# Optimization experiments

Hardware: AMD Instinct MI355X
Metric: run time of the kernel (lower is better)

Reference implementation:

```python
import jax, jax.numpy as jnp
import numpy as np

N_BUCKETS = 512
SLOTS_PER_BUCKET = 32
TAU = 0.1
ALPHA = 0.5


def _l2norm(x, eps=1e-12):
    return x / jnp.maximum(jnp.linalg.norm(x, axis=-1, keepdims=True), eps)


def setup_inputs() -> dict:
    key = jax.random.key(0)
    ks = jax.random.split(key, 6)
    B, T, D = 2, 2048, 1024
    total_slots = N_BUCKETS * SLOTS_PER_BUCKET
    vocab = 50257
    query_emb = jax.random.normal(ks[0], (B, T, D), dtype=jnp.float32)
    tids = jax.random.randint(ks[1], (B, T), 0, vocab)
    slot_keys = jax.random.normal(ks[2], (total_slots, D), dtype=jnp.float32)
    slot_values = jax.random.normal(ks[3], (total_slots, D), dtype=jnp.float32)
    slot_tids = jax.random.randint(ks[4], (total_slots,), 0, vocab)
    centroid_codebook = _l2norm(jax.random.normal(ks[5], (N_BUCKETS, D), dtype=jnp.float32))
    return {
        "query_emb": query_emb,
        "tids": tids,
        "slot_keys": slot_keys,
        "slot_values": slot_values,
        "slot_tids": slot_tids,
        "centroid_codebook": centroid_codebook,
    }


def reference(query_emb, tids, slot_keys, slot_values, slot_tids, centroid_codebook):
    # CentroidAddressableManifold.read
    buckets = tids % N_BUCKETS                                  # [B,T]
    lex_anchors = centroid_codebook[buckets]                    # [B,T,D]
    q_norm = _l2norm(query_emb)
    # bucket-indexed gather of 32 slots per token
    indices = buckets[..., None] * SLOTS_PER_BUCKET + jnp.arange(SLOTS_PER_BUCKET)  # [B,T,S]
    b_keys = slot_keys[indices]                                 # [B,T,S,D]
    b_vals = slot_values[indices]                               # [B,T,S,D]
    unified_query = _l2norm(ALPHA * q_norm + (1.0 - ALPHA) * lex_anchors)
    scores = jnp.einsum("btd,btsd->bts", unified_query, b_keys)  # [B,T,S]
    # hard-match path
    gathered_tids = slot_tids[indices]                          # [B,T,S]
    match_mask = (tids[..., None] == gathered_tids).astype(scores.dtype)
    match_sum = match_mask.sum(axis=-1, keepdims=True)
    has_match = match_sum > 0
    probs_hard = match_mask / (match_sum + 1e-9)
    probs_soft = jax.nn.softmax(scores / TAU, axis=-1)
    val_hard = jnp.einsum("bts,btsw->btw", probs_hard, b_vals)
    val_soft = jnp.einsum("bts,btsw->btw", probs_soft, b_vals)
    val_out = jnp.where(has_match, val_hard, val_soft)          # [B,T,D]
    return val_out
```

## Files before the change

### kernel.cpp

```cpp
#include <hip/hip_runtime.h>

#define NB 512
#define SLOTS 32
#define D 1024
#define D4 256
#define TC 16
#define CAP 64
#define TAU_INV 10.0f
#define BT 512

__global__ void k_zero(int* __restrict__ cnt) {
    if (threadIdx.x < NB) cnt[threadIdx.x] = 0;
}

__global__ void k_build(const int* __restrict__ tids, int n,
                        int* __restrict__ cnt, int* __restrict__ list) {
    int i = blockIdx.x * 256 + threadIdx.x;
    if (i < n) {
        int b = tids[i] & (NB - 1);
        int p = atomicAdd(&cnt[b], 1);
        if (p < CAP) list[b * CAP + p] = i;
    }
}

__global__ __launch_bounds__(BT, 2)
void k_main(const float* __restrict__ query,
            const int*   __restrict__ tids,
            const float* __restrict__ skeys,
            const float* __restrict__ svals,
            const int*   __restrict__ stids,
            const float* __restrict__ centroid,
            float*       __restrict__ out,
            const int*   __restrict__ cnt,
            const int*   __restrict__ list)
{
    const int bucket = blockIdx.x;
    const int tidx   = threadIdx.x;
    const int lane   = tidx & 63;
    const int wid    = tidx >> 6;

    const int count = min(cnt[bucket], CAP);
    if (count == 0) return;

    __shared__ float s_anchor[D];
    __shared__ float s_uq[TC][D];
    __shared__ float s_scores[TC][SLOTS];
    __shared__ float s_probs[TC][SLOTS];
    __shared__ int   s_tok[TC];
    __shared__ int   s_ttid[TC];

    if (tidx < D4)
        ((float4*)s_anchor)[tidx] = ((const float4*)centroid)[bucket * D4 + tidx];
    __syncthreads();

    for (int c0 = 0; c0 < count; c0 += TC) {
        const int nt = min(TC, count - c0);

        for (int t = wid; t < nt; t += 8) {
            const int tok = list[bucket * CAP + c0 + t];
            const float4* q4 = (const float4*)(query + (size_t)tok * D);
            float4 qv[4];
            float ss = 0.f;
            #pragma unroll
            for (int j = 0; j < 4; ++j) {
                qv[j] = q4[lane + 64 * j];
                ss += qv[j].x*qv[j].x + qv[j].y*qv[j].y + qv[j].z*qv[j].z + qv[j].w*qv[j].w;
            }
            #pragma unroll
            for (int off = 32; off >= 1; off >>= 1) ss += __shfl_xor(ss, off);
            const float qn = 0.5f / fmaxf(sqrtf(ss), 1e-12f);

            float4 uv[4];
            float ss2 = 0.f;
            #pragma unroll
            for (int j = 0; j < 4; ++j) {
                float4 av = ((const float4*)s_anchor)[lane + 64 * j];
                uv[j].x = qv[j].x * qn + 0.5f * av.x;
                uv[j].y = qv[j].y * qn + 0.5f * av.y;
                uv[j].z = qv[j].z * qn + 0.5f * av.z;
                uv[j].w = qv[j].w * qn + 0.5f * av.w;
                ss2 += uv[j].x*uv[j].x + uv[j].y*uv[j].y + uv[j].z*uv[j].z + uv[j].w*uv[j].w;
            }
            #pragma unroll
            for (int off = 32; off >= 1; off >>= 1) ss2 += __shfl_xor(ss2, off);
            const float un = 1.0f / fmaxf(sqrtf(ss2), 1e-12f);
            #pragma unroll
            for (int j = 0; j < 4; ++j) {
                float4 w4 = make_float4(uv[j].x*un, uv[j].y*un, uv[j].z*un, uv[j].w*un);
                ((float4*)s_uq[t])[lane + 64 * j] = w4;
            }
            if (lane == 0) { s_tok[t] = tok; s_ttid[t] = tids[tok]; }
        }
        __syncthreads();

        {
            const float4* kr = (const float4*)(skeys + ((size_t)bucket * SLOTS + wid * 4) * D);
            float4 k0[4], k1[4], k2[4], k3[4];
            #pragma unroll
            for (int j = 0; j < 4; ++j) {
                k0[j] = kr[0 * D4 + lane + 64 * j];
                k1[j] = kr[1 * D4 + lane + 64 * j];
                k2[j] = kr[2 * D4 + lane + 64 * j];
                k3[j] = kr[3 * D4 + lane + 64 * j];
            }
            for (int t = 0; t < nt; ++t) {
                const float4* u4 = (const float4*)s_uq[t];
                float P0 = 0.f, P1 = 0.f, P2 = 0.f, P3 = 0.f;
                #pragma unroll
                for (int j = 0; j < 4; ++j) {
                    float4 u = u4[lane + 64 * j];
                    P0 += k0[j].x*u.x + k0[j].y*u.y + k0[j].z*u.z + k0[j].w*u.w;
                    P1 += k1[j].x*u.x + k1[j].y*u.y + k1[j].z*u.z + k1[j].w*u.w;
                    P2 += k2[j].x*u.x + k2[j].y*u.y + k2[j].z*u.z + k2[j].w*u.w;
                    P3 += k3[j].x*u.x + k3[j].y*u.y + k3[j].z*u.z + k3[j].w*u.w;
                }
                {
                    const bool hi = (lane & 1) != 0;
                    const float sA = hi ? P0 : P2, kA = hi ? P2 : P0;
                    P0 = kA + __shfl_xor(sA, 1);
                    const float sB = hi ? P1 : P3, kB = hi ? P3 : P1;
                    P1 = kB + __shfl_xor(sB, 1);
                }
                {
                    const bool hi = (lane & 2) != 0;
                    const float sA = hi ? P0 : P1, kA = hi ? P1 : P0;
                    P0 = kA + __shfl_xor(sA, 2);
                }
                P0 += __shfl_xor(P0, 4);
                P0 += __shfl_xor(P0, 8);
                P0 += __shfl_xor(P0, 16);
                P0 += __shfl_xor(P0, 32);
                if (lane < 4)
                    s_scores[t][wid * 4 + (((lane & 1) << 1) | ((lane >> 1) & 1))] = P0;
            }
        }
        __syncthreads();

        for (int t = wid; t < nt; t += 8) {
            if (lane < 32) {
                const int s = lane;
                const float sc = s_scores[t][s];
                const int match = (stids[bucket * SLOTS + s] == s_ttid[t]) ? 1 : 0;
                float mx = sc;
                #pragma unroll
                for (int off = 16; off >= 1; off >>= 1) mx = fmaxf(mx, __shfl_xor(mx, off));
                const float e = __expf((sc - mx) * TAU_INV);
                float es = e;
                int   ms = match;
                #pragma unroll
                for (int off = 16; off >= 1; off >>= 1) {
                    es += __shfl_xor(es, off);
                    ms += __shfl_xor(ms, off);
                }
                float p;
                if (ms > 0) p = (float)match / ((float)ms + 1e-9f);
                else        p = e / es;
                s_probs[t][s] = p;
            }
        }
        __syncthreads();

        {
            const int col = tidx & 255;
            const int grp = tidx >> 8;
            float4 acc[TC];
            #pragma unroll
            for (int t = 0; t < TC; ++t) acc[t] = make_float4(0.f, 0.f, 0.f, 0.f);

            const float4* vb = (const float4*)(svals + ((size_t)bucket * SLOTS + grp * 16) * D);
            #pragma unroll
            for (int s0 = 0; s0 < 16; s0 += 8) {
                float4 v[8];
                #pragma unroll
                for (int i = 0; i < 8; ++i) v[i] = vb[(s0 + i) * D4 + col];
                #pragma unroll
                for (int t = 0; t < TC; ++t) {
                    if (t < nt) {
                        const float4 pA = ((const float4*)s_probs[t])[grp*4 + (s0>>3)*2 + 0];
                        const float4 pB = ((const float4*)s_probs[t])[grp*4 + (s0>>3)*2 + 1];
                        acc[t].x += pA.x*v[0].x + pA.y*v[1].x + pA.z*v[2].x + pA.w*v[3].x
                                  + pB.x*v[4].x + pB.y*v[5].x + pB.z*v[6].x + pB.w*v[7].x;
                        acc[t].y += pA.x*v[0].y + pA.y*v[1].y + pA.z*v[2].y + pA.w*v[3].y
                                  + pB.x*v[4].y + pB.y*v[5].y + pB.z*v[6].y + pB.w*v[7].y;
                        acc[t].z += pA.x*v[0].z + pA.y*v[1].z + pA.z*v[2].z + pA.w*v[3].z
                                  + pB.x*v[4].z + pB.y*v[5].z + pB.z*v[6].z + pB.w*v[7].z;
                        acc[t].w += pA.x*v[0].w + pA.y*v[1].w + pA.z*v[2].w + pA.w*v[3].w
                                  + pB.x*v[4].w + pB.y*v[5].w + pB.z*v[6].w + pB.w*v[7].w;
                    }
                }
            }
            if (grp == 0) {
                #pragma unroll
                for (int t = 0; t < TC; ++t)
                    if (t < nt) ((float4*)s_uq[t])[col] = acc[t];
            }
            __syncthreads();
            if (grp == 1) {
                #pragma unroll
                for (int t = 0; t < TC; ++t) {
                    if (t < nt) {
                        float4 b = ((float4*)s_uq[t])[col];
                        float4 r = make_float4(acc[t].x + b.x, acc[t].y + b.y,
                                               acc[t].z + b.z, acc[t].w + b.w);
                        ((float4*)(out + (size_t)s_tok[t] * D))[col] = r;
                    }
                }
            }
        }
        __syncthreads();
    }
}

extern "C" void kernel_launch(void* const* d_in, const int* in_sizes, int n_in,
                              void* d_out, int out_size, void* d_ws, size_t ws_size,
                              hipStream_t stream) {
    const float* query    = (const float*)d_in[0];
    const int*   tids     = (const int*)  d_in[1];
    const float* skeys    = (const float*)d_in[2];
    const float* svals    = (const float*)d_in[3];
    const int*   stids    = (const int*)  d_in[4];
    const float* centroid = (const float*)d_in[5];
    float* out = (float*)d_out;
    const int n_tokens = in_sizes[1];

    int* cnt  = (int*)d_ws;
    int* list = cnt + NB;

    k_zero<<<1, NB, 0, stream>>>(cnt);
    k_build<<<(n_tokens + 255) / 256, 256, 0, stream>>>(tids, n_tokens, cnt, list);
    k_main<<<NB, BT, 0, stream>>>(query, tids, skeys, svals, stids,
                                  centroid, out, cnt, list);
}
```

Baseline: 62.19 us.

## Split each bucket's tokens across two smaller blocks and drop cross-group reduction

Launches two 256-thread blocks per bucket, each handling alternate tokens of the bucket's list, with the token chunk reduced from 16 to 8. Each thread now accumulates all 32 slots for one column, which removes the shared-memory partial-sum exchange and its extra barrier. Anchors are read straight from global memory per token instead of being staged in shared memory. The intent is more blocks and better occupancy on a 256-CU part, at the cost of loading each bucket's keys and values twice and running two score rounds per chunk.

```diff
diff --git a/kernel.cpp b/kernel.cpp
--- a/kernel.cpp
+++ b/kernel.cpp
@@ -4,10 +4,10 @@
 #define SLOTS 32
 #define D 1024
 #define D4 256
-#define TC 16
+#define TC 8
 #define CAP 64
 #define TAU_INV 10.0f
-#define BT 512
+#define BT 256
 
 __global__ void k_zero(int* __restrict__ cnt) {
     if (threadIdx.x < NB) cnt[threadIdx.x] = 0;
@@ -34,51 +34,52 @@
             const int*   __restrict__ cnt,
             const int*   __restrict__ list)
 {
-    const int bucket = blockIdx.x;
+    const int bucket = blockIdx.x & (NB - 1);
+    const int part   = blockIdx.x >> 9;
     const int tidx   = threadIdx.x;
     const int lane   = tidx & 63;
     const int wid    = tidx >> 6;
 
     const int count = min(cnt[bucket], CAP);
-    if (count == 0) return;
-
-    __shared__ float s_anchor[D];
+    const int ncnt  = (count - part + 1) >> 1;
+    if (ncnt <= 0) return;
+
     __shared__ float s_uq[TC][D];
     __shared__ float s_scores[TC][SLOTS];
     __shared__ float s_probs[TC][SLOTS];
     __shared__ int   s_tok[TC];
     __shared__ int   s_ttid[TC];
 
-    if (tidx < D4)
-        ((float4*)s_anchor)[tidx] = ((const float4*)centroid)[bucket * D4 + tidx];
-    __syncthreads();
-
-    for (int c0 = 0; c0 < count; c0 += TC) {
-        const int nt = min(TC, count - c0);
-
-        for (int t = wid; t < nt; t += 8) {
-            const int tok = list[bucket * CAP + c0 + t];
+    const int slot_tid = stids[bucket * SLOTS + (lane & 31)];
+    const float4* kb = (const float4*)(skeys + (size_t)bucket * SLOTS * D);
+    const float4* vb = (const float4*)(svals + (size_t)bucket * SLOTS * D);
+    const float4* cb = (const float4*)(centroid + (size_t)bucket * D);
+
+    for (int c0 = 0; c0 < ncnt; c0 += TC) {
+        const int nt = min(TC, ncnt - c0);
+
+        for (int t = wid; t < nt; t += 4) {
+            const int tok = list[bucket * CAP + part + 2 * (c0 + t)];
             const float4* q4 = (const float4*)(query + (size_t)tok * D);
-            float4 qv[4];
+            float4 qv[4], anc[4];
             float ss = 0.f;
             #pragma unroll
             for (int j = 0; j < 4; ++j) {
-                qv[j] = q4[lane + 64 * j];
+                qv[j]  = q4[lane + 64 * j];
+                anc[j] = cb[lane + 64 * j];
                 ss += qv[j].x*qv[j].x + qv[j].y*qv[j].y + qv[j].z*qv[j].z + qv[j].w*qv[j].w;
             }
             #pragma unroll
             for (int off = 32; off >= 1; off >>= 1) ss += __shfl_xor(ss, off);
             const float qn = 0.5f / fmaxf(sqrtf(ss), 1e-12f);
-
             float4 uv[4];
             float ss2 = 0.f;
             #pragma unroll
             for (int j = 0; j < 4; ++j) {
-                float4 av = ((const float4*)s_anchor)[lane + 64 * j];
-                uv[j].x = qv[j].x * qn + 0.5f * av.x;
-                uv[j].y = qv[j].y * qn + 0.5f * av.y;
-                uv[j].z = qv[j].z * qn + 0.5f * av.z;
-                uv[j].w = qv[j].w * qn + 0.5f * av.w;
+                uv[j].x = qv[j].x * qn + 0.5f * anc[j].x;
+                uv[j].y = qv[j].y * qn + 0.5f * anc[j].y;
+                uv[j].z = qv[j].z * qn + 0.5f * anc[j].z;
+                uv[j].w = qv[j].w * qn + 0.5f * anc[j].w;
                 ss2 += uv[j].x*uv[j].x + uv[j].y*uv[j].y + uv[j].z*uv[j].z + uv[j].w*uv[j].w;
             }
             #pragma unroll
@@ -86,15 +87,17 @@
             const float un = 1.0f / fmaxf(sqrtf(ss2), 1e-12f);
             #pragma unroll
             for (int j = 0; j < 4; ++j) {
-                float4 w4 = make_float4(uv[j].x*un, uv[j].y*un, uv[j].z*un, uv[j].w*un);
-                ((float4*)s_uq[t])[lane + 64 * j] = w4;
+                ((float4*)s_uq[t])[lane + 64 * j] =
+                    make_float4(uv[j].x*un, uv[j].y*un, uv[j].z*un, uv[j].w*un);
             }
             if (lane == 0) { s_tok[t] = tok; s_ttid[t] = tids[tok]; }
         }
         __syncthreads();
 
-        {
-            const float4* kr = (const float4*)(skeys + ((size_t)bucket * SLOTS + wid * 4) * D);
+        #pragma unroll 1
+        for (int rnd = 0; rnd < 2; ++rnd) {
+            const int sbase = rnd * 16 + wid * 4;
+            const float4* kr = kb + (size_t)sbase * D4;
             float4 k0[4], k1[4], k2[4], k3[4];
             #pragma unroll
             for (int j = 0; j < 4; ++j) {
@@ -131,53 +134,45 @@
                 P0 += __shfl_xor(P0, 16);
                 P0 += __shfl_xor(P0, 32);
                 if (lane < 4)
-                    s_scores[t][wid * 4 + (((lane & 1) << 1) | ((lane >> 1) & 1))] = P0;
-            }
-        }
-        __syncthreads();
-
-        for (int t = wid; t < nt; t += 8) {
+                    s_scores[t][sbase + (((lane & 1) << 1) | ((lane >> 1) & 1))] = P0;
+            }
+        }
+        __syncthreads();
+
+        for (int t = wid; t < nt; t += 4) {
             if (lane < 32) {
-                const int s = lane;
-                const float sc = s_scores[t][s];
-                const int match = (stids[bucket * SLOTS + s] == s_ttid[t]) ? 1 : 0;
+                const float sc = s_scores[t][lane];
                 float mx = sc;
                 #pragma unroll
                 for (int off = 16; off >= 1; off >>= 1) mx = fmaxf(mx, __shfl_xor(mx, off));
                 const float e = __expf((sc - mx) * TAU_INV);
-                float es = e;
-                int   ms = match;
+                const float f = (slot_tid == s_ttid[t]) ? 1.f : 0.f;
+                float es = e, ms = f;
                 #pragma unroll
                 for (int off = 16; off >= 1; off >>= 1) {
                     es += __shfl_xor(es, off);
                     ms += __shfl_xor(ms, off);
                 }
-                float p;
-                if (ms > 0) p = (float)match / ((float)ms + 1e-9f);
-                else        p = e / es;
-                s_probs[t][s] = p;
+                s_probs[t][lane] = (ms > 0.f) ? f / (ms + 1e-9f) : e / es;
             }
         }
         __syncthreads();
 
         {
-            const int col = tidx & 255;
-            const int grp = tidx >> 8;
             float4 acc[TC];
             #pragma unroll
             for (int t = 0; t < TC; ++t) acc[t] = make_float4(0.f, 0.f, 0.f, 0.f);
 
-            const float4* vb = (const float4*)(svals + ((size_t)bucket * SLOTS + grp * 16) * D);
-            #pragma unroll
-            for (int s0 = 0; s0 < 16; s0 += 8) {
+            #pragma unroll 1
+            for (int s0 = 0; s0 < SLOTS; s0 += 8) {
                 float4 v[8];
                 #pragma unroll
-                for (int i = 0; i < 8; ++i) v[i] = vb[(s0 + i) * D4 + col];
+                for (int i = 0; i < 8; ++i) v[i] = vb[(s0 + i) * D4 + tidx];
                 #pragma unroll
                 for (int t = 0; t < TC; ++t) {
                     if (t < nt) {
-                        const float4 pA = ((const float4*)s_probs[t])[grp*4 + (s0>>3)*2 + 0];
-                        const float4 pB = ((const float4*)s_probs[t])[grp*4 + (s0>>3)*2 + 1];
+                        const float4 pA = ((const float4*)s_probs[t])[(s0 >> 2) + 0];
+                        const float4 pB = ((const float4*)s_probs[t])[(s0 >> 2) + 1];
                         acc[t].x += pA.x*v[0].x + pA.y*v[1].x + pA.z*v[2].x + pA.w*v[3].x
                                   + pB.x*v[4].x + pB.y*v[5].x + pB.z*v[6].x + pB.w*v[7].x;
                         acc[t].y += pA.x*v[0].y + pA.y*v[1].y + pA.z*v[2].y + pA.w*v[3].y
@@ -189,21 +184,10 @@
                     }
                 }
             }
-            if (grp == 0) {
-                #pragma unroll
-                for (int t = 0; t < TC; ++t)
-                    if (t < nt) ((float4*)s_uq[t])[col] = acc[t];
-            }
-            __syncthreads();
-            if (grp == 1) {
-                #pragma unroll
-                for (int t = 0; t < TC; ++t) {
-                    if (t < nt) {
-                        float4 b = ((float4*)s_uq[t])[col];
-                        float4 r = make_float4(acc[t].x + b.x, acc[t].y + b.y,
-                                               acc[t].z + b.z, acc[t].w + b.w);
-                        ((float4*)(out + (size_t)s_tok[t] * D))[col] = r;
-                    }
+            #pragma unroll
+            for (int t = 0; t < TC; ++t) {
+                if (t < nt) {
+                    ((float4*)(out + (size_t)s_tok[t] * D))[tidx] = acc[t];
                 }
             }
         }
@@ -226,8 +210,8 @@
     int* cnt  = (int*)d_ws;
     int* list = cnt + NB;
 
-    k_zero<<<1, NB, 0, stream>>>(cnt);
+    k_zero<<<1, 512, 0, stream>>>(cnt);
     k_build<<<(n_tokens + 255) / 256, 256, 0, stream>>>(tids, n_tokens, cnt, list);
-    k_main<<<NB, BT, 0, stream>>>(query, tids, skeys, svals, stids,
-                                  centroid, out, cnt, list);
-}
+    k_main<<<NB * 2, BT, 0, stream>>>(query, tids, skeys, svals, stids,
+                                      centroid, out, cnt, list);
+}
```

Measured after the change: 55.65 us. -10.5%, faster.
